# Kernel tuning notes

Measured on AMD Instinct MI355X. Metric: run time of the kernel, lower is better.

The kernel has to match this reference:

```python
import jax, jax.numpy as jnp
import numpy as np

EPS_RMS = 1e-6
EPS_SCALE = 1e-5


def setup_inputs() -> dict:
    key = jax.random.key(0)
    k1, k2 = jax.random.split(key)
    B, S, D_IN, D_OUT = 4, 2048, 2048, 8192
    x = jax.random.normal(k1, (B, S, D_IN), dtype=jnp.float32)
    # kaiming_uniform-ish init bound
    bound = 1.0 / np.sqrt(D_IN)
    weight = jax.random.uniform(k2, (D_OUT, D_IN), dtype=jnp.float32, minval=-bound, maxval=bound)
    gamma = jnp.ones((D_IN,), dtype=jnp.float32)
    return {"x": x, "weight": weight, "gamma": gamma}


def rmsnorm(x, gamma):
    xf = x.astype(jnp.float32)
    inv = jax.lax.rsqrt(jnp.mean(xf * xf, axis=-1, keepdims=True) + EPS_RMS)
    return (xf * inv).astype(x.dtype) * gamma


def quantize_weights_ternary(weight):
    scale = jnp.maximum(jnp.mean(jnp.abs(weight)), EPS_SCALE)
    wn = weight / scale
    wq = jax.lax.stop_gradient(jnp.round(jnp.clip(wn, -1.0, 1.0)) - wn) + wn  # STE
    return wq, scale


def reference(x, weight, gamma):
    x_norm = rmsnorm(x, gamma)                      # [B, S, D_in]
    wq, scale = quantize_weights_ternary(weight)    # [D_out, D_in], scalar
    out = jnp.einsum('bsd,od->bso', x_norm, wq)     # [B, S, D_out]
    return out * scale
```

## Files before the change

### kernel.cpp

```cpp
#include <hip/hip_runtime.h>
#include <hip/hip_bf16.h>
#include <stdint.h>

#define M_ROWS 8192
#define K_DIM  2048
#define N_DIM  8192
#define W_ELEMS (N_DIM * K_DIM)
#define X_ELEMS (M_ROWS * K_DIM)

typedef __bf16 v8bf __attribute__((ext_vector_type(8)));
typedef float  v4f  __attribute__((ext_vector_type(4)));

__device__ inline unsigned short f2bf(float f) {
  uint32_t u = __builtin_bit_cast(uint32_t, f);
  uint32_t r = (u + 0x7fffu + ((u >> 16) & 1u)) >> 16;
  return (unsigned short)r;
}

__device__ inline void async_copy16(const void* g, void* l) {
  __builtin_amdgcn_global_load_lds(
      (const __attribute__((address_space(1))) void*)g,
      (__attribute__((address_space(3))) void*)l, 16, 0, 0);
}

__global__ __launch_bounds__(256) void absum_kernel(const float* __restrict__ W,
                                                    double* __restrict__ out) {
  int tid = blockIdx.x * 256 + threadIdx.x;
  int stride = gridDim.x * 256;
  const float4* W4 = (const float4*)W;
  const int n4 = W_ELEMS / 4;
  double acc = 0.0;
  for (int i = tid; i < n4; i += stride) {
    float4 v = W4[i];
    acc += (double)fabsf(v.x) + (double)fabsf(v.y) +
           (double)fabsf(v.z) + (double)fabsf(v.w);
  }
  for (int off = 32; off > 0; off >>= 1) acc += __shfl_down(acc, off);
  __shared__ double wsum[4];
  int lane = threadIdx.x & 63, wid = threadIdx.x >> 6;
  if (lane == 0) wsum[wid] = acc;
  __syncthreads();
  if (threadIdx.x == 0) atomicAdd(out, wsum[0] + wsum[1] + wsum[2] + wsum[3]);
}

__global__ __launch_bounds__(256) void rmsnorm_kernel(const float* __restrict__ X,
                                                      const float* __restrict__ gamma,
                                                      unsigned short* __restrict__ Xn) {
  const int row = blockIdx.x;
  const int t = threadIdx.x;
  const float4* xr = (const float4*)(X + (size_t)row * K_DIM);
  float4 a = xr[t * 2];
  float4 b = xr[t * 2 + 1];
  float ss = a.x * a.x + a.y * a.y + a.z * a.z + a.w * a.w +
             b.x * b.x + b.y * b.y + b.z * b.z + b.w * b.w;
  for (int off = 32; off > 0; off >>= 1) ss += __shfl_down(ss, off);
  __shared__ float wsum[4];
  int lane = t & 63, wid = t >> 6;
  if (lane == 0) wsum[wid] = ss;
  __syncthreads();
  float total = wsum[0] + wsum[1] + wsum[2] + wsum[3];
  float inv = 1.0f / sqrtf(total * (1.0f / (float)K_DIM) + 1e-6f);
  const float4* gr = (const float4*)gamma;
  float4 g0 = gr[t * 2];
  float4 g1 = gr[t * 2 + 1];
  union { unsigned short h[8]; uint4 u; } p;
  p.h[0] = f2bf((a.x * inv) * g0.x);
  p.h[1] = f2bf((a.y * inv) * g0.y);
  p.h[2] = f2bf((a.z * inv) * g0.z);
  p.h[3] = f2bf((a.w * inv) * g0.w);
  p.h[4] = f2bf((b.x * inv) * g1.x);
  p.h[5] = f2bf((b.y * inv) * g1.y);
  p.h[6] = f2bf((b.z * inv) * g1.z);
  p.h[7] = f2bf((b.w * inv) * g1.w);
  ((uint4*)(Xn + (size_t)row * K_DIM))[t] = p.u;
}

__global__ __launch_bounds__(256) void quant_kernel(const float* __restrict__ W,
                                                    const double* __restrict__ sum_ws,
                                                    unsigned short* __restrict__ Wq) {
  float s = (float)fmax(sum_ws[0] * (1.0 / (double)W_ELEMS), 1e-5);
  size_t idx = ((size_t)blockIdx.x * 256 + threadIdx.x) * 8;
  const float4* w4 = (const float4*)(W + idx);
  float4 a = w4[0];
  float4 b = w4[1];
  union { unsigned short h[8]; uint4 u; } p;
  p.h[0] = f2bf(rintf(fminf(1.f, fmaxf(-1.f, a.x / s))));
  p.h[1] = f2bf(rintf(fminf(1.f, fmaxf(-1.f, a.y / s))));
  p.h[2] = f2bf(rintf(fminf(1.f, fmaxf(-1.f, a.z / s))));
  p.h[3] = f2bf(rintf(fminf(1.f, fmaxf(-1.f, a.w / s))));
  p.h[4] = f2bf(rintf(fminf(1.f, fmaxf(-1.f, b.x / s))));
  p.h[5] = f2bf(rintf(fminf(1.f, fmaxf(-1.f, b.y / s))));
  p.h[6] = f2bf(rintf(fminf(1.f, fmaxf(-1.f, b.z / s))));
  p.h[7] = f2bf(rintf(fminf(1.f, fmaxf(-1.f, b.w / s))));
  *(uint4*)(Wq + idx) = p.u;
}

__global__ __launch_bounds__(256, 3) void gemm_kernel(
    const unsigned short* __restrict__ A,
    const unsigned short* __restrict__ B,
    const double* __restrict__ sum_ws,
    float* __restrict__ C) {
  __shared__ __align__(16) unsigned short lds_a[128 * 64];
  __shared__ __align__(16) unsigned short lds_b[128 * 64];

  const int tid = threadIdx.x;
  const int lane = tid & 63;
  const int wave = tid >> 6;

  const int lin = blockIdx.x;
  const int wi = lin & 15;
  const int st = lin >> 4;
  const int mb = (st >> 4) * 4 + (wi >> 2);
  const int nb = (st & 15) * 4 + (wi & 3);
  const int m0 = mb * 128;
  const int n0 = nb * 128;
  const int wm = (wave & 1) * 64;
  const int wn = (wave >> 1) * 64;

  const float s = (float)fmax(sum_ws[0] * (1.0 / (double)W_ELEMS), 1e-5);

  v4f acc[4][4] = {};

  const int srow_in = lane >> 3;
  const int scg = (lane & 7) ^ (srow_in & 7);

  for (int k0 = 0; k0 < K_DIM; k0 += 64) {
#pragma unroll
    for (int j = 0; j < 4; ++j) {
      const int chunk = wave * 4 + j;
      const int row = chunk * 8 + srow_in;
      const unsigned short* ga = A + (size_t)(m0 + row) * K_DIM + (k0 + scg * 8);
      async_copy16(ga, (char*)lds_a + chunk * 1024);
      const unsigned short* gb = B + (size_t)(n0 + row) * K_DIM + (k0 + scg * 8);
      async_copy16(gb, (char*)lds_b + chunk * 1024);
    }
    __syncthreads();

#pragma unroll
    for (int sub = 0; sub < 2; ++sub) {
      v8bf af[4], bfr[4];
      const int kg = sub * 4 + (lane >> 4);
#pragma unroll
      for (int t = 0; t < 4; ++t) {
        const int arow = wm + t * 16 + (lane & 15);
        af[t] = *(const v8bf*)((const char*)lds_a + arow * 128 + ((kg ^ (arow & 7)) << 4));
        const int brow = wn + t * 16 + (lane & 15);
        bfr[t] = *(const v8bf*)((const char*)lds_b + brow * 128 + ((kg ^ (brow & 7)) << 4));
      }
#pragma unroll
      for (int tm = 0; tm < 4; ++tm)
#pragma unroll
        for (int tn = 0; tn < 4; ++tn)
          acc[tm][tn] = __builtin_amdgcn_mfma_f32_16x16x32_bf16(
              bfr[tn], af[tm], acc[tm][tn], 0, 0, 0);
    }
    __syncthreads();
  }

  const int mcol = m0 + wm + (lane & 15);
  const int nrow = n0 + wn + (lane >> 4) * 4;
#pragma unroll
  for (int tm = 0; tm < 4; ++tm) {
#pragma unroll
    for (int tn = 0; tn < 4; ++tn) {
      const int m = mcol + tm * 16;
      const int n = nrow + tn * 16;
      float4 v;
      v.x = acc[tm][tn][0] * s;
      v.y = acc[tm][tn][1] * s;
      v.z = acc[tm][tn][2] * s;
      v.w = acc[tm][tn][3] * s;
      *(float4*)&C[(size_t)m * N_DIM + n] = v;
    }
  }
}

extern "C" void kernel_launch(void* const* d_in, const int* in_sizes, int n_in,
                              void* d_out, int out_size, void* d_ws, size_t ws_size,
                              hipStream_t stream) {
  const float* x = (const float*)d_in[0];
  const float* w = (const float*)d_in[1];
  const float* gamma = (const float*)d_in[2];
  float* out = (float*)d_out;

  double* ws_sum = (double*)d_ws;
  unsigned short* xn = (unsigned short*)((char*)d_ws + 16);
  unsigned short* wq = (unsigned short*)((char*)d_ws + 16 + (size_t)X_ELEMS * 2);

  hipMemsetAsync(d_ws, 0, 16, stream);
  absum_kernel<<<2048, 256, 0, stream>>>(w, ws_sum);
  rmsnorm_kernel<<<M_ROWS, 256, 0, stream>>>(x, gamma, xn);
  quant_kernel<<<W_ELEMS / (256 * 8), 256, 0, stream>>>(w, ws_sum, wq);
  gemm_kernel<<<4096, 256, 0, stream>>>(xn, wq, ws_sum, out);
}
```

Measured before the change: 713.1 us.

## Rewrite GEMM as 256x256 tile, 8-wave, double-buffered pipelined kernel

Replaces the 128x128 single-buffered GEMM with 256x256 block tiles computed by 8 waves (512 threads), each wave owning a 128x64 sub-tile. LDS is double-buffered into half-tiles, and async global-to-LDS loads for the next K-tiles are interleaved with MFMA work using explicit barriers, vmcnt waits and s_setprio. The block index is remapped with an XCD-aware swizzle. This aims to hide memory latency and raise arithmetic intensity, at the cost of 128KB of LDS, higher register pressure and delicate hand-written synchronization.

After: 619.2 us. 13.2% less time.

```diff
diff --git a/kernel.cpp b/kernel.cpp
--- a/kernel.cpp
+++ b/kernel.cpp
@@ -7,6 +7,7 @@
 #define N_DIM  8192
 #define W_ELEMS (N_DIM * K_DIM)
 #define X_ELEMS (M_ROWS * K_DIM)
+#define NT 32
 
 typedef __bf16 v8bf __attribute__((ext_vector_type(8)));
 typedef float  v4f  __attribute__((ext_vector_type(4)));
@@ -95,84 +96,165 @@
   *(uint4*)(Wq + idx) = p.u;
 }
 
-__global__ __launch_bounds__(256, 3) void gemm_kernel(
+__global__ __launch_bounds__(512, 2) void gemm_kernel(
     const unsigned short* __restrict__ A,
     const unsigned short* __restrict__ B,
     const double* __restrict__ sum_ws,
     float* __restrict__ C) {
-  __shared__ __align__(16) unsigned short lds_a[128 * 64];
-  __shared__ __align__(16) unsigned short lds_b[128 * 64];
+  __shared__ __align__(16) char lds[131072];
 
   const int tid = threadIdx.x;
   const int lane = tid & 63;
   const int wave = tid >> 6;
-
-  const int lin = blockIdx.x;
-  const int wi = lin & 15;
-  const int st = lin >> 4;
-  const int mb = (st >> 4) * 4 + (wi >> 2);
-  const int nb = (st & 15) * 4 + (wi & 3);
-  const int m0 = mb * 128;
-  const int n0 = nb * 128;
-  const int wm = (wave & 1) * 64;
-  const int wn = (wave >> 1) * 64;
+  const int wm = wave & 1;
+  const int wn = wave >> 1;
+
+  const int bid = blockIdx.x;
+  const int swz = (bid & 7) * 128 + (bid >> 3);
+  const int st = swz >> 4, wi = swz & 15;
+  const int mb = (st >> 3) * 4 + (wi >> 2);
+  const int nb = (st & 7) * 4 + (wi & 3);
+  const int m0 = mb * 256;
+  const int n0 = nb * 256;
+
+  const int srow3 = lane >> 3;
+  const int scg = (lane & 7) ^ srow3;
+
+  const int aoff_a = wm * 8192 + (lane & 15) * 128;
+  const int boff_b = wn * 4096 + (lane & 15) * 128;
+  const int swzk0 = ((lane >> 4) ^ (lane & 7)) << 4;
+  const int swzk1 = ((4 + (lane >> 4)) ^ (lane & 7)) << 4;
+
+  v4f acc[8][4] = {};
+  v8bf af[4][2];
+  v8bf b0f[2][2];
+  v8bf b1f[2][2];
+
+#define STAGE_A(B_, H_, KT_) do {                                              \
+    _Pragma("unroll")                                                          \
+    for (int j = 0; j < 2; ++j) {                                              \
+      const int chunk_ = wave * 2 + j;                                         \
+      const int slot_ = chunk_ * 8 + srow3;                                    \
+      const int row_ = ((slot_ >> 6) << 7) + ((H_) << 6) + (slot_ & 63);       \
+      async_copy16(A + (size_t)(m0 + row_) * K_DIM + ((KT_) << 6) + (scg << 3),\
+                   lds + (B_) * 32768 + (H_) * 16384 + chunk_ * 1024);         \
+    } } while (0)
+
+#define STAGE_B(B_, H_, KT_) do {                                              \
+    _Pragma("unroll")                                                          \
+    for (int j = 0; j < 2; ++j) {                                              \
+      const int chunk_ = wave * 2 + j;                                         \
+      const int slot_ = chunk_ * 8 + srow3;                                    \
+      const int row_ = ((slot_ >> 5) << 6) + ((H_) << 5) + (slot_ & 31);       \
+      async_copy16(B + (size_t)(n0 + row_) * K_DIM + ((KT_) << 6) + (scg << 3),\
+                   lds + 65536 + (B_) * 32768 + (H_) * 16384 + chunk_ * 1024); \
+    } } while (0)
+
+#define LOADA(B_, QM_) do {                                                    \
+    _Pragma("unroll")                                                          \
+    for (int tm = 0; tm < 4; ++tm) {                                           \
+      af[tm][0] = *(const v8bf*)(lds + (B_) * 32768 + (QM_) * 16384 +          \
+                                 aoff_a + tm * 2048 + swzk0);                  \
+      af[tm][1] = *(const v8bf*)(lds + (B_) * 32768 + (QM_) * 16384 +          \
+                                 aoff_a + tm * 2048 + swzk1);                  \
+    } } while (0)
+
+#define LOADB(B_, QN_, DST) do {                                               \
+    _Pragma("unroll")                                                          \
+    for (int tn = 0; tn < 2; ++tn) {                                           \
+      DST[tn][0] = *(const v8bf*)(lds + 65536 + (B_) * 32768 + (QN_) * 16384 + \
+                                  boff_b + tn * 2048 + swzk0);                 \
+      DST[tn][1] = *(const v8bf*)(lds + 65536 + (B_) * 32768 + (QN_) * 16384 + \
+                                  boff_b + tn * 2048 + swzk1);                 \
+    } } while (0)
+
+#define MMAC(BF, QM_, QN_) do {                                                \
+    _Pragma("unroll")                                                          \
+    for (int ks = 0; ks < 2; ++ks)                                             \
+    _Pragma("unroll")                                                          \
+    for (int tm = 0; tm < 4; ++tm)                                             \
+    _Pragma("unroll")                                                          \
+    for (int tn = 0; tn < 2; ++tn)                                             \
+      acc[(QM_) * 4 + tm][(QN_) * 2 + tn] =                                    \
+          __builtin_amdgcn_mfma_f32_16x16x32_bf16(                             \
+              BF[tn][ks], af[tm][ks],                                          \
+              acc[(QM_) * 4 + tm][(QN_) * 2 + tn], 0, 0, 0);                   \
+  } while (0)
+
+#define BARRIER() __builtin_amdgcn_s_barrier()
+#define VM8() asm volatile("s_waitcnt vmcnt(8)" ::: "memory")
+
+#define TILE(T_, B_) do {                                                      \
+    const int t1_ = ((T_) + 1 < NT) ? (T_) + 1 : NT - 1;                       \
+    const int t2_ = ((T_) + 2 < NT) ? (T_) + 2 : NT - 1;                       \
+                                                            \
+    LOADA(B_, 0);                                                              \
+    LOADB(B_, 0, b0f);                                                         \
+    STAGE_B(1 - (B_), 1, t1_);                                                 \
+    BARRIER();                                                                 \
+    __builtin_amdgcn_s_setprio(1); MMAC(b0f, 0, 0);                            \
+    __builtin_amdgcn_s_setprio(0);                                             \
+    VM8(); BARRIER();                                                          \
+                                                            \
+    LOADB(B_, 1, b1f);                                                         \
+    STAGE_A(1 - (B_), 1, t1_);                                                 \
+    BARRIER();                                                                 \
+    __builtin_amdgcn_s_setprio(1); MMAC(b1f, 0, 1);                            \
+    __builtin_amdgcn_s_setprio(0);                                             \
+    VM8(); BARRIER();                                                          \
+                                                            \
+    LOADA(B_, 1);                                                              \
+    STAGE_A(B_, 0, t2_);                                                       \
+    BARRIER();                                                                 \
+    __builtin_amdgcn_s_setprio(1); MMAC(b0f, 1, 0);                            \
+    __builtin_amdgcn_s_setprio(0);                                             \
+    BARRIER();                                                                 \
+                                                            \
+    STAGE_B(B_, 0, t2_);                                                       \
+    BARRIER();                                                                 \
+    __builtin_amdgcn_s_setprio(1); MMAC(b1f, 1, 1);                            \
+    __builtin_amdgcn_s_setprio(0);                                             \
+    VM8(); BARRIER();                                                          \
+  } while (0)
+
+  STAGE_A(0, 0, 0);
+  STAGE_B(0, 0, 0);
+  STAGE_B(0, 1, 0);
+  STAGE_A(0, 1, 0);
+  STAGE_A(1, 0, 1);
+  STAGE_B(1, 0, 1);
+  VM8();
+  BARRIER();
+
+  for (int t = 0; t < NT; t += 2) {
+    TILE(t, 0);
+    TILE(t + 1, 1);
+  }
 
   const float s = (float)fmax(sum_ws[0] * (1.0 / (double)W_ELEMS), 1e-5);
-
-  v4f acc[4][4] = {};
-
-  const int srow_in = lane >> 3;
-  const int scg = (lane & 7) ^ (srow_in & 7);
-
-  for (int k0 = 0; k0 < K_DIM; k0 += 64) {
+  const int mBase = m0 + wm * 128 + (lane & 15);
+  const int nBase = n0 + wn * 64 + ((lane >> 4) << 2);
 #pragma unroll
-    for (int j = 0; j < 4; ++j) {
-      const int chunk = wave * 4 + j;
-      const int row = chunk * 8 + srow_in;
-      const unsigned short* ga = A + (size_t)(m0 + row) * K_DIM + (k0 + scg * 8);
-      async_copy16(ga, (char*)lds_a + chunk * 1024);
-      const unsigned short* gb = B + (size_t)(n0 + row) * K_DIM + (k0 + scg * 8);
-      async_copy16(gb, (char*)lds_b + chunk * 1024);
-    }
-    __syncthreads();
-
-#pragma unroll
-    for (int sub = 0; sub < 2; ++sub) {
-      v8bf af[4], bfr[4];
-      const int kg = sub * 4 + (lane >> 4);
-#pragma unroll
-      for (int t = 0; t < 4; ++t) {
-        const int arow = wm + t * 16 + (lane & 15);
-        af[t] = *(const v8bf*)((const char*)lds_a + arow * 128 + ((kg ^ (arow & 7)) << 4));
-        const int brow = wn + t * 16 + (lane & 15);
-        bfr[t] = *(const v8bf*)((const char*)lds_b + brow * 128 + ((kg ^ (brow & 7)) << 4));
-      }
-#pragma unroll
-      for (int tm = 0; tm < 4; ++tm)
-#pragma unroll
-        for (int tn = 0; tn < 4; ++tn)
-          acc[tm][tn] = __builtin_amdgcn_mfma_f32_16x16x32_bf16(
-              bfr[tn], af[tm], acc[tm][tn], 0, 0, 0);
-    }
-    __syncthreads();
-  }
-
-  const int mcol = m0 + wm + (lane & 15);
-  const int nrow = n0 + wn + (lane >> 4) * 4;
-#pragma unroll
-  for (int tm = 0; tm < 4; ++tm) {
+  for (int tm = 0; tm < 8; ++tm) {
 #pragma unroll
     for (int tn = 0; tn < 4; ++tn) {
-      const int m = mcol + tm * 16;
-      const int n = nrow + tn * 16;
       float4 v;
       v.x = acc[tm][tn][0] * s;
       v.y = acc[tm][tn][1] * s;
       v.z = acc[tm][tn][2] * s;
       v.w = acc[tm][tn][3] * s;
-      *(float4*)&C[(size_t)m * N_DIM + n] = v;
+      *(float4*)&C[(size_t)(mBase + tm * 16) * N_DIM + (nBase + tn * 16)] = v;
     }
   }
+
+#undef STAGE_A
+#undef STAGE_B
+#undef LOADA
+#undef LOADB
+#undef MMAC
+#undef BARRIER
+#undef VM8
+#undef TILE
 }
 
 extern "C" void kernel_launch(void* const* d_in, const int* in_sizes, int n_in,
@@ -191,5 +273,5 @@
   absum_kernel<<<2048, 256, 0, stream>>>(w, ws_sum);
   rmsnorm_kernel<<<M_ROWS, 256, 0, stream>>>(x, gamma, xn);
   quant_kernel<<<W_ELEMS / (256 * 8), 256, 0, stream>>>(w, ws_sum, wq);
-  gemm_kernel<<<4096, 256, 0, stream>>>(xn, wq, ws_sum, out);
-}
+  gemm_kernel<<<(M_ROWS / 256) * (N_DIM / 256), 512, 0, stream>>>(xn, wq, ws_sum, out);
+}
```
